# Kernel optimization log

Hardware: AMD Instinct MI355X
Metric: run time of the kernel (lower is better)

Reference implementation:

```python
import jax, jax.numpy as jnp
import numpy as np
from jax import lax
from jax.scipy.special import logsumexp

NUM_CLASSES = 170
ALPHA = 0.2
B, T = 16, 8192


def setup_inputs() -> dict:
    key = jax.random.key(0)
    logits = jax.random.normal(key, (B, T, NUM_CLASSES), dtype=jnp.float32)
    # transition matrix: alpha on diagonal, uniform off-diagonal
    off = (1.0 - ALPHA) / (NUM_CLASSES - 1)
    trans = jnp.full((NUM_CLASSES, NUM_CLASSES), off, dtype=jnp.float32)
    trans = trans.at[jnp.arange(NUM_CLASSES), jnp.arange(NUM_CLASSES)].set(ALPHA)
    init = jnp.full((NUM_CLASSES,), 1.0 / NUM_CLASSES, dtype=jnp.float32)
    return {"logits": logits, "transition_matrix": trans, "initial_distribution": init}


def reference(logits, transition_matrix, initial_distribution):
    eps = 1e-12
    log_T = jnp.log(transition_matrix + eps)          # (C, C)
    log_init = jnp.log(initial_distribution + eps)    # (C,)
    log_probs = jax.nn.log_softmax(logits, axis=-1)   # (B, T, C)
    Bn, Tn, C = log_probs.shape
    lp = jnp.moveaxis(log_probs, 1, 0)                # (T, B, C) time-major for scan

    # forward recursion: alpha_t[j] = logsumexp_i(alpha_{t-1}[i] + logT[i,j]) + lp_t[j]
    alpha0 = log_init[None, :] + lp[0]                # (B, C)

    def fwd_step(a_prev, lp_t):
        a = logsumexp(a_prev[:, :, None] + log_T[None, :, :], axis=1) + lp_t
        return a, a

    _, alpha_rest = lax.scan(fwd_step, alpha0, lp[1:])
    alpha = jnp.concatenate([alpha0[None], alpha_rest], axis=0)  # (T, B, C)

    # backward recursion: beta_t[i] = logsumexp_j(logT[i,j] + lp_{t+1}[j] + beta_{t+1}[j])
    betaT = jnp.zeros((Bn, C), dtype=log_probs.dtype)

    def bwd_step(b_next, lp_next):
        b = logsumexp(log_T[None, :, :] + (lp_next + b_next)[:, None, :], axis=2)
        return b, b

    _, beta_rest = lax.scan(bwd_step, betaT, lp[1:], reverse=True)
    beta = jnp.concatenate([beta_rest, betaT[None]], axis=0)     # (T, B, C)

    posterior = jax.nn.softmax(alpha + beta, axis=-1)            # (T, B, C)
    return jnp.moveaxis(posterior, 0, 1)                         # (B, T, C)
```

## Files before the change

### kernel.cpp

```cpp
#include <hip/hip_runtime.h>
#include <hip/hip_fp16.h>


#define NCLS 170
#define BB 16
#define TT 8192
#define LCH 32
#define WARM 16
#define NCHUNK (TT / LCH)
#define P2S 44

typedef float f32x2 __attribute__((ext_vector_type(2)));

struct Row { f32x2 xy; float z; };

__device__ __forceinline__ float wave_sum_b(float x) {
  x += __int_as_float(__builtin_amdgcn_update_dpp(0, __float_as_int(x), 0x111, 0xF, 0xF, true));
  x += __int_as_float(__builtin_amdgcn_update_dpp(0, __float_as_int(x), 0x112, 0xF, 0xF, true));
  x += __int_as_float(__builtin_amdgcn_update_dpp(0, __float_as_int(x), 0x114, 0xF, 0xF, true));
  x += __int_as_float(__builtin_amdgcn_update_dpp(0, __float_as_int(x), 0x118, 0xF, 0xF, true));
  x += __int_as_float(__builtin_amdgcn_update_dpp(0, __float_as_int(x), 0x142, 0xA, 0xF, true));
  x += __int_as_float(__builtin_amdgcn_update_dpp(0, __float_as_int(x), 0x143, 0xC, 0xF, true));
  return __int_as_float(__builtin_amdgcn_readlane(__float_as_int(x), 63));
}

__global__ __launch_bounds__(128, 4) void hmm_fb(const float* __restrict__ logits,
                                                 const float* __restrict__ trans,
                                                 const float* __restrict__ initd,
                                                 float* __restrict__ out) {
  __shared__ __half2 p01[LCH * 64];
  __shared__ __half  p2s[LCH * P2S];
  const int lane = threadIdx.x & 63;
  const int w = threadIdx.x >> 6;

  const int d = blockIdx.x;
  const int o = (d & 7) * (BB * NCHUNK / 8) + (d >> 3);
  const int b = o / NCHUNK;
  const int chunk = o % NCHUNK;
  const int t0 = chunk * LCH;
  const int t1 = t0 + LCH;

  const float off = trans[1] + 1e-12f;
  const float dia = trans[0] + 1e-12f;
  const float dd = dia - off;
  const f32x2 dd2 = {dd, dd};

  const bool cok = (lane < NCLS - 128);
  const float* lg = logits + (size_t)b * TT * NCLS;

  auto ldraw = [&](int t) -> Row {
    const float* r = lg + (size_t)t * NCLS;
    Row wv;
    wv.xy = *(const f32x2*)(r + 2 * lane);
    wv.z = cok ? r[128 + lane] : 0.f;
    return wv;
  };
  auto eRow = [&](const Row& wv) -> Row {
    Row e;
    e.xy.x = __expf(wv.xy.x);
    e.xy.y = __expf(wv.xy.y);
    e.z = cok ? __expf(wv.z) : 0.f;
    return e;
  };

  Row a0, a1, a2, a3, b0, b1, b2, b3;
  f32x2 q01 = {1.f, 1.f};
  float q2 = cok ? 1.f : 0.f;

  auto ldB = [&](int tp1) -> Row {
    int rr = tp1 < 0 ? 0 : (tp1 > TT - 1 ? TT - 1 : tp1);
    Row wv = ldraw(rr);
    if (tp1 >= TT) { wv.xy.x = 0.f; wv.xy.y = 0.f; wv.z = 0.f; }
    return wv;
  };

  if (w == 0) {
    f32x2 v01; float v2s;
    auto fcore = [&](const Row& e, f32x2& u01, float& u2) -> float {
      u01 = v01 * e.xy;
      u2 = v2s * e.z;
      float S = wave_sum_b(u01.x + u01.y + u2);
      float os = off * S;
      f32x2 os2 = {os, os};
      v01 = dd2 * u01 + os2;
      v2s = __fmaf_rn(dd, u2, os);
      return S;
    };

    int ts;
    if (t0 == 0) {
      ts = 0;
      v01 = *(const f32x2*)(initd + 2 * lane);
      v2s = cok ? initd[128 + lane] : 0.f;
    } else {
      ts = t0 - WARM;
      v01.x = 1.f; v01.y = 1.f; v2s = cok ? 1.f : 0.f;
    }
    a0 = ldraw(ts); a1 = ldraw(ts + 1); a2 = ldraw(ts + 2); a3 = ldraw(ts + 3);
    b0 = ldraw(ts + 4); b1 = ldraw(ts + 5); b2 = ldraw(ts + 6); b3 = ldraw(ts + 7);

    for (int gg = 0; gg < (t0 - ts) / 4; ++gg) {
      const int tn = ts + 8 + 4 * gg;
      Row n0 = ldraw(tn), n1 = ldraw(tn + 1), n2 = ldraw(tn + 2), n3 = ldraw(tn + 3);
      Row e0 = eRow(a0), e1 = eRow(a1), e2 = eRow(a2), e3 = eRow(a3);
      f32x2 u01; float u2;
      fcore(e0, u01, u2);
      fcore(e1, u01, u2);
      fcore(e2, u01, u2);
      float S3 = fcore(e3, u01, u2);
      float rs = __builtin_amdgcn_rcpf(S3);
      f32x2 rs2 = {rs, rs};
      v01 = v01 * rs2; v2s *= rs;
      a0 = b0; a1 = b1; a2 = b2; a3 = b3;
      b0 = n0; b1 = n1; b2 = n2; b3 = n3;
    }

#define FSTORE(st, u01v, u2v, xr)                                              \
    p01[(st) * 64 + lane] = __floats2half2_rn(u01v.x * xr, u01v.y * xr);       \
    if (cok) p2s[(st) * P2S + lane] = __float2half(u2v * xr);

#define FGROUP(i)                                                              \
  {                                                                            \
    const int tn = t0 + (i) + 8;                                               \
    Row n0 = ldraw(tn + 0 > t1 - 1 ? t1 - 1 : tn + 0);                         \
    Row n1 = ldraw(tn + 1 > t1 - 1 ? t1 - 1 : tn + 1);                         \
    Row n2 = ldraw(tn + 2 > t1 - 1 ? t1 - 1 : tn + 2);                         \
    Row n3 = ldraw(tn + 3 > t1 - 1 ? t1 - 1 : tn + 3);                         \
    Row e0 = eRow(a0), e1 = eRow(a1), e2 = eRow(a2), e3 = eRow(a3);            \
    f32x2 u01; float u2;                                                       \
    float S0 = fcore(e0, u01, u2);                                             \
    float x0 = __builtin_amdgcn_rcpf(S0);                                      \
    FSTORE((i) + 0, u01, u2, x0)                                               \
    float S1 = fcore(e1, u01, u2);                                             \
    float x1 = __builtin_amdgcn_rcpf(S1);                                      \
    FSTORE((i) + 1, u01, u2, x1)                                               \
    float S2 = fcore(e2, u01, u2);                                             \
    float x2 = __builtin_amdgcn_rcpf(S2);                                      \
    FSTORE((i) + 2, u01, u2, x2)                                               \
    float S3 = fcore(e3, u01, u2);                                             \
    float x3 = __builtin_amdgcn_rcpf(S3);                                      \
    FSTORE((i) + 3, u01, u2, x3)                                               \
    f32x2 x32 = {x3, x3};                                                      \
    v01 = v01 * x32; v2s *= x3;             \
    a0 = b0; a1 = b1; a2 = b2; a3 = b3;                                        \
    b0 = n0; b1 = n1; b2 = n2; b3 = n3;                                        \
  }

    FGROUP(0) FGROUP(4) FGROUP(8) FGROUP(12)
    FGROUP(16) FGROUP(20) FGROUP(24) FGROUP(28)
#undef FGROUP
#undef FSTORE
  } else {
    auto bcore = [&](const Row& e) -> float {
      f32x2 w01 = e.xy * q01;
      float w2 = e.z * q2;
      float S = wave_sum_b(w01.x + w01.y + w2);
      float os = off * S;
      f32x2 os2 = {os, os};
      q01 = dd2 * w01 + os2;
      q2 = __fmaf_rn(dd, w2, os);
      return S;
    };

    int te2 = t1 + WARM;
    if (te2 > TT) te2 = TT;
    const int tstart = te2 - 1;

    a0 = ldB(tstart + 1); a1 = ldB(tstart); a2 = ldB(tstart - 1); a3 = ldB(tstart - 2);
    b0 = ldB(tstart - 3); b1 = ldB(tstart - 4); b2 = ldB(tstart - 5); b3 = ldB(tstart - 6);

    for (int gg = 0; gg < (te2 - t1) / 4; ++gg) {
      const int tp = tstart - 7 - 4 * gg;
      Row n0 = ldB(tp), n1 = ldB(tp - 1), n2 = ldB(tp - 2), n3 = ldB(tp - 3);
      Row e0 = eRow(a0), e1 = eRow(a1), e2 = eRow(a2), e3 = eRow(a3);
      bcore(e0); bcore(e1); bcore(e2);
      float S3 = bcore(e3);
      float rs = __builtin_amdgcn_rcpf(S3);
      f32x2 rs2 = {rs, rs};
      q01 = q01 * rs2; q2 *= rs;
      a0 = b0; a1 = b1; a2 = b2; a3 = b3;
      b0 = n0; b1 = n1; b2 = n2; b3 = n3;
    }
  }

  __syncthreads();

  if (w == 1) {
    auto bcore = [&](const Row& e) -> float {
      f32x2 w01 = e.xy * q01;
      float w2 = e.z * q2;
      float S = wave_sum_b(w01.x + w01.y + w2);
      float os = off * S;
      f32x2 os2 = {os, os};
      q01 = dd2 * w01 + os2;
      q2 = __fmaf_rn(dd, w2, os);
      return S;
    };

#define WPOST(tt, ta)                                                          \
  {                                                                            \
    __half2 h01 = p01[(tt) * 64 + lane];                                       \
    f32x2 p01v; p01v.x = __low2float(h01); p01v.y = __high2float(h01);         \
    f32x2 a01 = p01v * q01;                                                    \
    float p2f = 0.f;                                                           \
    if (cok) p2f = __half2float(p2s[(tt) * P2S + lane]);                       \
    float g2 = p2f * q2;                                                       \
    float z = wave_sum_b(a01.x + a01.y + g2);                                  \
    float iz = __builtin_amdgcn_rcpf(z);                                       \
    f32x2 iz2 = {iz, iz};                                                      \
    float* op = out + ((size_t)b * TT + (ta)) * NCLS;                          \
    f32x2 o01 = a01 * iz2;                                                     \
    __builtin_nontemporal_store(o01, (f32x2*)(op + 2 * lane));                 \
    if (cok) __builtin_nontemporal_store(g2 * iz, op + 128 + lane);            \
  }

#define BGROUP(i)                                                              \
  {                                                                            \
    const int tp = t1 - 8 - (i);                  \
    Row n0 = ldB(tp + 0 < t0 + 1 ? t0 + 1 : tp + 0);                           \
    Row n1 = ldB(tp - 1 < t0 + 1 ? t0 + 1 : tp - 1);                           \
    Row n2 = ldB(tp - 2 < t0 + 1 ? t0 + 1 : tp - 2);                           \
    Row n3 = ldB(tp - 3 < t0 + 1 ? t0 + 1 : tp - 3);                           \
    Row e0 = eRow(a0), e1 = eRow(a1), e2 = eRow(a2), e3 = eRow(a3);            \
    const int t = t1 - 1 - (i);                                                \
    bcore(e0); WPOST(LCH - 1 - (i), t)                                         \
    bcore(e1); WPOST(LCH - 2 - (i), t - 1)                                     \
    bcore(e2); WPOST(LCH - 3 - (i), t - 2)                                     \
    float S3 = bcore(e3); WPOST(LCH - 4 - (i), t - 3)                          \
    float rs = __builtin_amdgcn_rcpf(S3);                                      \
    f32x2 rs2 = {rs, rs};                                                      \
    q01 = q01 * rs2; q2 *= rs;                                                 \
    a0 = b0; a1 = b1; a2 = b2; a3 = b3;                                        \
    b0 = n0; b1 = n1; b2 = n2; b3 = n3;                                        \
  }

    BGROUP(0) BGROUP(4) BGROUP(8) BGROUP(12)
    BGROUP(16) BGROUP(20) BGROUP(24) BGROUP(28)
#undef BGROUP
#undef WPOST
  }
}

extern "C" void kernel_launch(void* const* d_in, const int* in_sizes, int n_in,
                              void* d_out, int out_size, void* d_ws, size_t ws_size,
                              hipStream_t stream) {
  const float* logits = (const float*)d_in[0];
  const float* trans  = (const float*)d_in[1];
  const float* initd  = (const float*)d_in[2];
  float* out = (float*)d_out;
  dim3 grid(BB * NCHUNK);
  dim3 block(128);
  hipLaunchKernelGGL(hmm_fb, grid, block, 0, stream, logits, trans, initd, out);
}
```

Measured before the change: 71.77 us.

## Run forward and backward serially in one wave with shorter chunks

Each block now uses a single 64-lane wave that runs the forward warm-up and pass, then the backward warm-up and pass, instead of two waves that split forward and backward with a barrier. The chunk length drops from 32 to 16, which doubles the grid and the share of warm-up work relative to useful steps. The prefetch depth shrinks from two groups of four rows to one, and the nontemporal output stores become plain stores. The aim is more concurrent blocks and less register and LDS pressure per block, at the cost of serialised per-block latency and more redundant warm-up loads and exps.

```diff
diff --git a/kernel.cpp b/kernel.cpp
--- a/kernel.cpp
+++ b/kernel.cpp
@@ -5,7 +5,7 @@
 #define NCLS 170
 #define BB 16
 #define TT 8192
-#define LCH 32
+#define LCH 16
 #define WARM 16
 #define NCHUNK (TT / LCH)
 #define P2S 44
@@ -24,14 +24,13 @@
   return __int_as_float(__builtin_amdgcn_readlane(__float_as_int(x), 63));
 }
 
-__global__ __launch_bounds__(128, 4) void hmm_fb(const float* __restrict__ logits,
+__global__ __launch_bounds__(64, 10) void hmm_fb(const float* __restrict__ logits,
                                                  const float* __restrict__ trans,
                                                  const float* __restrict__ initd,
                                                  float* __restrict__ out) {
   __shared__ __half2 p01[LCH * 64];
   __shared__ __half  p2s[LCH * P2S];
-  const int lane = threadIdx.x & 63;
-  const int w = threadIdx.x >> 6;
+  const int lane = threadIdx.x;
 
   const int d = blockIdx.x;
   const int o = (d & 7) * (BB * NCHUNK / 8) + (d >> 3);
@@ -63,57 +62,44 @@
     return e;
   };
 
-  Row a0, a1, a2, a3, b0, b1, b2, b3;
-  f32x2 q01 = {1.f, 1.f};
-  float q2 = cok ? 1.f : 0.f;
-
-  auto ldB = [&](int tp1) -> Row {
-    int rr = tp1 < 0 ? 0 : (tp1 > TT - 1 ? TT - 1 : tp1);
-    Row wv = ldraw(rr);
-    if (tp1 >= TT) { wv.xy.x = 0.f; wv.xy.y = 0.f; wv.z = 0.f; }
-    return wv;
-  };
-
-  if (w == 0) {
-    f32x2 v01; float v2s;
-    auto fcore = [&](const Row& e, f32x2& u01, float& u2) -> float {
-      u01 = v01 * e.xy;
-      u2 = v2s * e.z;
-      float S = wave_sum_b(u01.x + u01.y + u2);
-      float os = off * S;
-      f32x2 os2 = {os, os};
-      v01 = dd2 * u01 + os2;
-      v2s = __fmaf_rn(dd, u2, os);
-      return S;
-    };
-
-    int ts;
-    if (t0 == 0) {
-      ts = 0;
-      v01 = *(const f32x2*)(initd + 2 * lane);
-      v2s = cok ? initd[128 + lane] : 0.f;
-    } else {
-      ts = t0 - WARM;
-      v01.x = 1.f; v01.y = 1.f; v2s = cok ? 1.f : 0.f;
-    }
-    a0 = ldraw(ts); a1 = ldraw(ts + 1); a2 = ldraw(ts + 2); a3 = ldraw(ts + 3);
-    b0 = ldraw(ts + 4); b1 = ldraw(ts + 5); b2 = ldraw(ts + 6); b3 = ldraw(ts + 7);
-
-    for (int gg = 0; gg < (t0 - ts) / 4; ++gg) {
-      const int tn = ts + 8 + 4 * gg;
-      Row n0 = ldraw(tn), n1 = ldraw(tn + 1), n2 = ldraw(tn + 2), n3 = ldraw(tn + 3);
-      Row e0 = eRow(a0), e1 = eRow(a1), e2 = eRow(a2), e3 = eRow(a3);
-      f32x2 u01; float u2;
-      fcore(e0, u01, u2);
-      fcore(e1, u01, u2);
-      fcore(e2, u01, u2);
-      float S3 = fcore(e3, u01, u2);
-      float rs = __builtin_amdgcn_rcpf(S3);
-      f32x2 rs2 = {rs, rs};
-      v01 = v01 * rs2; v2s *= rs;
-      a0 = b0; a1 = b1; a2 = b2; a3 = b3;
-      b0 = n0; b1 = n1; b2 = n2; b3 = n3;
-    }
+  f32x2 v01; float v2s;
+  auto fcore = [&](const Row& e, f32x2& u01, float& u2) -> float {
+    u01 = v01 * e.xy;
+    u2 = v2s * e.z;
+    float S = wave_sum_b(u01.x + u01.y + u2);
+    float os = off * S;
+    f32x2 os2 = {os, os};
+    v01 = dd2 * u01 + os2;
+    v2s = __fmaf_rn(dd, u2, os);
+    return S;
+  };
+
+  Row r0, r1, r2, r3;
+  int ts;
+  if (t0 == 0) {
+    ts = 0;
+    v01 = *(const f32x2*)(initd + 2 * lane);
+    v2s = cok ? initd[128 + lane] : 0.f;
+  } else {
+    ts = t0 - WARM;
+    v01.x = 1.f; v01.y = 1.f; v2s = cok ? 1.f : 0.f;
+  }
+  r0 = ldraw(ts); r1 = ldraw(ts + 1); r2 = ldraw(ts + 2); r3 = ldraw(ts + 3);
+
+  for (int gg = 0; gg < (t0 - ts) / 4; ++gg) {
+    const int tn = ts + 4 + 4 * gg;
+    Row n0 = ldraw(tn), n1 = ldraw(tn + 1), n2 = ldraw(tn + 2), n3 = ldraw(tn + 3);
+    Row e0 = eRow(r0), e1 = eRow(r1), e2 = eRow(r2), e3 = eRow(r3);
+    f32x2 u01; float u2;
+    fcore(e0, u01, u2);
+    fcore(e1, u01, u2);
+    fcore(e2, u01, u2);
+    float S3 = fcore(e3, u01, u2);
+    float rs = __builtin_amdgcn_rcpf(S3);
+    f32x2 rs2 = {rs, rs};
+    v01 = v01 * rs2; v2s *= rs;
+    r0 = n0; r1 = n1; r2 = n2; r3 = n3;
+  }
 
 #define FSTORE(st, u01v, u2v, xr)                                              \
     p01[(st) * 64 + lane] = __floats2half2_rn(u01v.x * xr, u01v.y * xr);       \
@@ -121,12 +107,12 @@
 
 #define FGROUP(i)                                                              \
   {                                                                            \
-    const int tn = t0 + (i) + 8;                                               \
+    const int tn = t0 + (i) + 4;                                               \
     Row n0 = ldraw(tn + 0 > t1 - 1 ? t1 - 1 : tn + 0);                         \
     Row n1 = ldraw(tn + 1 > t1 - 1 ? t1 - 1 : tn + 1);                         \
     Row n2 = ldraw(tn + 2 > t1 - 1 ? t1 - 1 : tn + 2);                         \
     Row n3 = ldraw(tn + 3 > t1 - 1 ? t1 - 1 : tn + 3);                         \
-    Row e0 = eRow(a0), e1 = eRow(a1), e2 = eRow(a2), e3 = eRow(a3);            \
+    Row e0 = eRow(r0), e1 = eRow(r1), e2 = eRow(r2), e3 = eRow(r3);            \
     f32x2 u01; float u2;                                                       \
     float S0 = fcore(e0, u01, u2);                                             \
     float x0 = __builtin_amdgcn_rcpf(S0);                                      \
@@ -142,60 +128,49 @@
     FSTORE((i) + 3, u01, u2, x3)                                               \
     f32x2 x32 = {x3, x3};                                                      \
     v01 = v01 * x32; v2s *= x3;             \
-    a0 = b0; a1 = b1; a2 = b2; a3 = b3;                                        \
-    b0 = n0; b1 = n1; b2 = n2; b3 = n3;                                        \
-  }
-
-    FGROUP(0) FGROUP(4) FGROUP(8) FGROUP(12)
-    FGROUP(16) FGROUP(20) FGROUP(24) FGROUP(28)
+    r0 = n0; r1 = n1; r2 = n2; r3 = n3;                                        \
+  }
+
+  FGROUP(0) FGROUP(4) FGROUP(8) FGROUP(12)
 #undef FGROUP
 #undef FSTORE
-  } else {
-    auto bcore = [&](const Row& e) -> float {
-      f32x2 w01 = e.xy * q01;
-      float w2 = e.z * q2;
-      float S = wave_sum_b(w01.x + w01.y + w2);
-      float os = off * S;
-      f32x2 os2 = {os, os};
-      q01 = dd2 * w01 + os2;
-      q2 = __fmaf_rn(dd, w2, os);
-      return S;
-    };
-
-    int te2 = t1 + WARM;
-    if (te2 > TT) te2 = TT;
-    const int tstart = te2 - 1;
-
-    a0 = ldB(tstart + 1); a1 = ldB(tstart); a2 = ldB(tstart - 1); a3 = ldB(tstart - 2);
-    b0 = ldB(tstart - 3); b1 = ldB(tstart - 4); b2 = ldB(tstart - 5); b3 = ldB(tstart - 6);
-
-    for (int gg = 0; gg < (te2 - t1) / 4; ++gg) {
-      const int tp = tstart - 7 - 4 * gg;
-      Row n0 = ldB(tp), n1 = ldB(tp - 1), n2 = ldB(tp - 2), n3 = ldB(tp - 3);
-      Row e0 = eRow(a0), e1 = eRow(a1), e2 = eRow(a2), e3 = eRow(a3);
-      bcore(e0); bcore(e1); bcore(e2);
-      float S3 = bcore(e3);
-      float rs = __builtin_amdgcn_rcpf(S3);
-      f32x2 rs2 = {rs, rs};
-      q01 = q01 * rs2; q2 *= rs;
-      a0 = b0; a1 = b1; a2 = b2; a3 = b3;
-      b0 = n0; b1 = n1; b2 = n2; b3 = n3;
-    }
-  }
-
-  __syncthreads();
-
-  if (w == 1) {
-    auto bcore = [&](const Row& e) -> float {
-      f32x2 w01 = e.xy * q01;
-      float w2 = e.z * q2;
-      float S = wave_sum_b(w01.x + w01.y + w2);
-      float os = off * S;
-      f32x2 os2 = {os, os};
-      q01 = dd2 * w01 + os2;
-      q2 = __fmaf_rn(dd, w2, os);
-      return S;
-    };
+
+  f32x2 q01 = {1.f, 1.f};
+  float q2 = cok ? 1.f : 0.f;
+  int te2 = t1 + WARM;
+  if (te2 > TT) te2 = TT;
+  const int tstart = te2 - 1;
+
+  auto ldB = [&](int tp1) -> Row {
+    int rr = tp1 < 0 ? 0 : (tp1 > TT - 1 ? TT - 1 : tp1);
+    Row wv = ldraw(rr);
+    if (tp1 >= TT) { wv.xy.x = 0.f; wv.xy.y = 0.f; wv.z = 0.f; }
+    return wv;
+  };
+  auto bcore = [&](const Row& e) -> float {
+    f32x2 w01 = e.xy * q01;
+    float w2 = e.z * q2;
+    float S = wave_sum_b(w01.x + w01.y + w2);
+    float os = off * S;
+    f32x2 os2 = {os, os};
+    q01 = dd2 * w01 + os2;
+    q2 = __fmaf_rn(dd, w2, os);
+    return S;
+  };
+
+  r0 = ldB(tstart + 1); r1 = ldB(tstart); r2 = ldB(tstart - 1); r3 = ldB(tstart - 2);
+
+  for (int gg = 0; gg < (te2 - t1) / 4; ++gg) {
+    const int t = tstart - 4 * gg;
+    Row n0 = ldB(t - 3), n1 = ldB(t - 4), n2 = ldB(t - 5), n3 = ldB(t - 6);
+    Row e0 = eRow(r0), e1 = eRow(r1), e2 = eRow(r2), e3 = eRow(r3);
+    bcore(e0); bcore(e1); bcore(e2);
+    float S3 = bcore(e3);
+    float rs = __builtin_amdgcn_rcpf(S3);
+    f32x2 rs2 = {rs, rs};
+    q01 = q01 * rs2; q2 *= rs;
+    r0 = n0; r1 = n1; r2 = n2; r3 = n3;
+  }
 
 #define WPOST(tt, ta)                                                          \
   {                                                                            \
@@ -210,19 +185,18 @@
     f32x2 iz2 = {iz, iz};                                                      \
     float* op = out + ((size_t)b * TT + (ta)) * NCLS;                          \
     f32x2 o01 = a01 * iz2;                                                     \
-    __builtin_nontemporal_store(o01, (f32x2*)(op + 2 * lane));                 \
-    if (cok) __builtin_nontemporal_store(g2 * iz, op + 128 + lane);            \
+    *(f32x2*)(op + 2 * lane) = o01;                                            \
+    if (cok) op[128 + lane] = g2 * iz;                                         \
   }
 
 #define BGROUP(i)                                                              \
   {                                                                            \
-    const int tp = t1 - 8 - (i);                  \
-    Row n0 = ldB(tp + 0 < t0 + 1 ? t0 + 1 : tp + 0);                           \
-    Row n1 = ldB(tp - 1 < t0 + 1 ? t0 + 1 : tp - 1);                           \
-    Row n2 = ldB(tp - 2 < t0 + 1 ? t0 + 1 : tp - 2);                           \
-    Row n3 = ldB(tp - 3 < t0 + 1 ? t0 + 1 : tp - 3);                           \
-    Row e0 = eRow(a0), e1 = eRow(a1), e2 = eRow(a2), e3 = eRow(a3);            \
     const int t = t1 - 1 - (i);                                                \
+    Row n0 = ldB(t - 3 < t0 + 1 ? t0 + 1 : t - 3);                             \
+    Row n1 = ldB(t - 4 < t0 + 1 ? t0 + 1 : t - 4);                             \
+    Row n2 = ldB(t - 5 < t0 + 1 ? t0 + 1 : t - 5);                             \
+    Row n3 = ldB(t - 6 < t0 + 1 ? t0 + 1 : t - 6);                             \
+    Row e0 = eRow(r0), e1 = eRow(r1), e2 = eRow(r2), e3 = eRow(r3);            \
     bcore(e0); WPOST(LCH - 1 - (i), t)                                         \
     bcore(e1); WPOST(LCH - 2 - (i), t - 1)                                     \
     bcore(e2); WPOST(LCH - 3 - (i), t - 2)                                     \
@@ -230,15 +204,12 @@
     float rs = __builtin_amdgcn_rcpf(S3);                                      \
     f32x2 rs2 = {rs, rs};                                                      \
     q01 = q01 * rs2; q2 *= rs;                                                 \
-    a0 = b0; a1 = b1; a2 = b2; a3 = b3;                                        \
-    b0 = n0; b1 = n1; b2 = n2; b3 = n3;                                        \
-  }
-
-    BGROUP(0) BGROUP(4) BGROUP(8) BGROUP(12)
-    BGROUP(16) BGROUP(20) BGROUP(24) BGROUP(28)
+    r0 = n0; r1 = n1; r2 = n2; r3 = n3;                                        \
+  }
+
+  BGROUP(0) BGROUP(4) BGROUP(8) BGROUP(12)
 #undef BGROUP
 #undef WPOST
-  }
 }
 
 extern "C" void kernel_launch(void* const* d_in, const int* in_sizes, int n_in,
@@ -249,6 +220,6 @@
   const float* initd  = (const float*)d_in[2];
   float* out = (float*)d_out;
   dim3 grid(BB * NCHUNK);
-  dim3 block(128);
+  dim3 block(64);
   hipLaunchKernelGGL(hmm_fb, grid, block, 0, stream, logits, trans, initd, out);
 }
```

After: 72.42 us. About the same (+0.9%).
